# Optimization experiments

Hardware: AMD Instinct MI355X
Metric: run time of the kernel (lower is better)

Reference implementation:

```python
import jax, jax.numpy as jnp
import numpy as np

B, S, DMODEL, HEADS = 2, 2048, 1024, 16
DK = DMODEL // HEADS
DV = DMODEL // HEADS


def setup_inputs() -> dict:
    key = jax.random.key(0)
    kx, kq, kk, kv = jax.random.split(key, 4)
    x = jax.random.normal(kx, (B, S, DMODEL), dtype=jnp.float32)
    # stacked per-head projection weights, shape [H, dmodel, dk/dv]
    # (equivalent to nn.Linear(dmodel, dk, bias=False) per head)
    scale = 1.0 / np.sqrt(DMODEL)
    Wq = jax.random.uniform(kq, (HEADS, DMODEL, DK), jnp.float32, -scale, scale)
    Wk = jax.random.uniform(kk, (HEADS, DMODEL, DK), jnp.float32, -scale, scale)
    Wv = jax.random.uniform(kv, (HEADS, DMODEL, DV), jnp.float32, -scale, scale)
    return {"x": x, "Wq": Wq, "Wk": Wk, "Wv": Wv}


def reference(x, Wq, Wk, Wv):
    # per-head projections, batched across heads: [B,H,S,dk]
    q = jnp.einsum("bsd,hdk->bhsk", x, Wq)
    k = jnp.einsum("bsd,hdk->bhsk", x, Wk)
    v = jnp.einsum("bsd,hdv->bhsv", x, Wv)
    # NOTE: original module applies NO 1/sqrt(dk) scaling — keep faithful
    scores = jnp.einsum("bhqk,bhsk->bhqs", q, k)  # [B,H,S,S]
    attn = jax.nn.softmax(scores, axis=-1)
    out = jnp.einsum("bhqs,bhsv->bhqv", attn, v)  # [B,H,S,dv]
    # concat heads along last dim in head order
    Bsz, H, Sq, Dv = out.shape
    return jnp.transpose(out, (0, 2, 1, 3)).reshape(Bsz, Sq, H * Dv)
```

## Files before the change

kernel.cpp:

```cpp
#include <hip/hip_runtime.h>

#define B_ 2
#define S_ 2048
#define D_ 1024
#define H_ 16
#define DK_ 64
#define M_ (B_ * S_)
#define N_ (3 * D_)

typedef __bf16 bf16x8 __attribute__((ext_vector_type(8)));
typedef short s8vec __attribute__((ext_vector_type(8)));
typedef float f4vec __attribute__((ext_vector_type(4)));

static __device__ __forceinline__ ushort f2b(float f) {
  union { float f; unsigned u; } v; v.f = f;
  unsigned u = v.u;
  u += 0x7FFFu + ((u >> 16) & 1u);
  return (ushort)(u >> 16);
}

static __device__ __forceinline__ unsigned pk2(float a, float b) {
#if __has_builtin(__builtin_amdgcn_cvt_pk_bf16_f32)
  typedef __bf16 b2 __attribute__((ext_vector_type(2)));
  b2 r = __builtin_amdgcn_cvt_pk_bf16_f32(a, b);
  return __builtin_bit_cast(unsigned, r);
#else
  return (unsigned)f2b(a) | ((unsigned)f2b(b) << 16);
#endif
}

static __device__ __forceinline__ float exp2f_fast(float x) {
#if __has_builtin(__builtin_amdgcn_exp2f)
  return __builtin_amdgcn_exp2f(x);
#else
  return __expf(x * 0.6931471805599453f);
#endif
}

static __device__ __forceinline__ f4vec mfma16(s8vec a, s8vec b, f4vec c) {
  return __builtin_amdgcn_mfma_f32_16x16x32_bf16(
      __builtin_bit_cast(bf16x8, a), __builtin_bit_cast(bf16x8, b), c, 0, 0, 0);
}

static __device__ __forceinline__ void gl_lds16(const ushort* g, ushort* l) {
  __builtin_amdgcn_global_load_lds(
      (const __attribute__((address_space(1))) unsigned*)g,
      (__attribute__((address_space(3))) unsigned*)l, 16, 0, 0);
}

static __device__ __forceinline__ void wg_barrier_lds() {
  asm volatile("" ::: "memory");
  __builtin_amdgcn_s_waitcnt(0xC07F);
  __builtin_amdgcn_s_barrier();
  asm volatile("" ::: "memory");
}

__global__ __launch_bounds__(256) void cvt_xw(const float* __restrict__ x,
                                              const float* __restrict__ Wq,
                                              const float* __restrict__ Wk,
                                              const float* __restrict__ Wv,
                                              ushort* __restrict__ xb,
                                              ushort* __restrict__ wbt) {
  __shared__ ushort T[64 * 72];
  const int t = threadIdx.x;
  if (blockIdx.x < 4096) {
    int i = blockIdx.x * 256 + t;
    float4 v = ((const float4*)x)[i];
    ushort4 o;
    o.x = f2b(v.x); o.y = f2b(v.y); o.z = f2b(v.z); o.w = f2b(v.w);
    ((ushort4*)xb)[i] = o;
    return;
  }
  const int r = blockIdx.x - 4096;
  const int w = r >> 8, h = (r >> 4) & 15, d0 = (r & 15) * 64;
  const float* W = (w == 0) ? Wq : (w == 1) ? Wk : Wv;
  const float sc = (w == 0) ? 1.4426950408889634f : 1.0f;
  const float* src = W + (size_t)h * 65536 + (size_t)d0 * 64;
#pragma unroll
  for (int j = 0; j < 4; ++j) {
    int idx = j * 256 + t;
    int dr = idx >> 4, kc = (idx & 15) * 4;
    float4 v = *(const float4*)(src + dr * 64 + kc);
    T[(kc + 0) * 72 + dr] = f2b(v.x * sc);
    T[(kc + 1) * 72 + dr] = f2b(v.y * sc);
    T[(kc + 2) * 72 + dr] = f2b(v.z * sc);
    T[(kc + 3) * 72 + dr] = f2b(v.w * sc);
  }
  __syncthreads();
  const int kk = t >> 2, dcg = (t & 3) * 16;
  ushort* dst = wbt + ((size_t)w * 1024 + h * 64 + kk) * 1024 + d0 + dcg;
  *(s8vec*)dst       = *(const s8vec*)&T[kk * 72 + dcg];
  *(s8vec*)(dst + 8) = *(const s8vec*)&T[kk * 72 + dcg + 8];
}

__global__ __launch_bounds__(256) void proj_gemm(const ushort* __restrict__ xb,
                                                 const ushort* __restrict__ wbt,
                                                 ushort* __restrict__ qkv) {
  __shared__ __attribute__((aligned(16))) ushort As[128 * 64];
  __shared__ __attribute__((aligned(16))) ushort Bs[128 * 64];
  const int tid = threadIdx.x, wid = tid >> 6, lane = tid & 63;
  const int quad = lane >> 4, l15 = lane & 15;
  const int wm = wid & 1, wn = wid >> 1;
  const int m0 = blockIdx.x * 128, n0 = blockIdx.y * 128;

  f4vec acc[4][4];
#pragma unroll
  for (int mb = 0; mb < 4; mb++)
#pragma unroll
    for (int nb = 0; nb < 4; nb++)
#pragma unroll
      for (int i = 0; i < 4; i++) acc[mb][nb][i] = 0.f;

  const int sr = tid >> 3, sg = tid & 7;
  const int lg = sg ^ (sr & 7);
  const ushort* Ab = xb + (size_t)m0 * D_;
  const ushort* Bb = wbt + (size_t)n0 * D_;

  for (int k0 = 0; k0 < D_; k0 += 64) {
    __syncthreads();
#pragma unroll
    for (int j = 0; j < 4; ++j) {
      int r = j * 32 + sr;
      gl_lds16(Ab + (size_t)r * D_ + k0 + lg * 8, &As[j * 2048 + wid * 512]);
      gl_lds16(Bb + (size_t)r * D_ + k0 + lg * 8, &Bs[j * 2048 + wid * 512]);
    }
    __syncthreads();

#pragma unroll
    for (int kb = 0; kb < 2; ++kb) {
      s8vec af[4], bf[4];
#pragma unroll
      for (int mb = 0; mb < 4; ++mb) {
        int m = wm * 64 + mb * 16 + l15;
        int gpos = (kb * 4 + quad) ^ (m & 7);
        af[mb] = *(const s8vec*)&As[m * 64 + gpos * 8];
      }
#pragma unroll
      for (int nb = 0; nb < 4; ++nb) {
        int n = wn * 64 + nb * 16 + l15;
        int gpos = (kb * 4 + quad) ^ (n & 7);
        bf[nb] = *(const s8vec*)&Bs[n * 64 + gpos * 8];
      }
#pragma unroll
      for (int mb = 0; mb < 4; ++mb)
#pragma unroll
        for (int nb = 0; nb < 4; ++nb)
          acc[mb][nb] = mfma16(af[mb], bf[nb], acc[mb][nb]);
    }
  }

  const size_t per = (size_t)B_ * H_ * S_ * DK_;
  const int w = n0 >> 10;
  if (w == 2) {
    ushort* vt = qkv + 2 * per;
#pragma unroll
    for (int mb = 0; mb < 4; ++mb)
#pragma unroll
      for (int nb = 0; nb < 4; ++nb)
#pragma unroll
        for (int i = 0; i < 4; ++i) {
          int m = m0 + wm * 64 + mb * 16 + quad * 4 + i;
          int b = m >> 11, s = m & 2047;
          int n1 = (n0 & 1023) + wn * 64 + nb * 16 + l15;
          vt[((size_t)b * 1024 + n1) * S_ + s] = f2b(acc[mb][nb][i]);
        }
  } else {
#pragma unroll
    for (int mb = 0; mb < 4; ++mb)
#pragma unroll
      for (int nb = 0; nb < 4; ++nb)
#pragma unroll
        for (int i = 0; i < 4; ++i) {
          int m = m0 + wm * 64 + mb * 16 + quad * 4 + i;
          int b = m >> 11, s = m & 2047;
          int n1 = (n0 & 1023) + wn * 64 + nb * 16 + l15;
          qkv[(size_t)w * per + (((size_t)b * H_ + (n1 >> 6)) * S_ + s) * 64 + (n1 & 63)] =
              f2b(acc[mb][nb][i]);
        }
  }
}

__global__ __launch_bounds__(256) void attn(const ushort* __restrict__ qg,
                                            const ushort* __restrict__ kg,
                                            const ushort* __restrict__ vtg,
                                            float* __restrict__ out) {
  __shared__ __attribute__((aligned(16))) ushort Ks[128 * 64];
  __shared__ __attribute__((aligned(16))) ushort Vt[2][64 * 64];
  const int qt = blockIdx.x, bh = blockIdx.y;
  const int b = bh >> 4, h = bh & 15;
  const int tid = threadIdx.x, wid = tid >> 6, lane = tid & 63;
  const int quad = lane >> 4, l15 = lane & 15, l7 = l15 & 7;

  const ushort* qbase = qg + ((size_t)bh * S_ + qt * 128 + wid * 32) * DK_;
  s8vec bq[2][2];
#pragma unroll
  for (int qb = 0; qb < 2; ++qb)
#pragma unroll
    for (int kc = 0; kc < 2; ++kc)
      bq[qb][kc] = *(const s8vec*)(qbase + (size_t)(qb * 16 + l15) * DK_ + kc * 32 + quad * 8);

  f4vec o[4][2];
  float lsum[2] = {0.f, 0.f};
#pragma unroll
  for (int nb = 0; nb < 4; ++nb)
#pragma unroll
    for (int qb = 0; qb < 2; ++qb)
#pragma unroll
      for (int i = 0; i < 4; ++i) o[nb][qb][i] = 0.f;

  const int r5 = tid >> 3, gs = tid & 7;
  const int gk = gs ^ (r5 & 7);
  const ushort* kb_ = kg + (size_t)bh * S_ * DK_;
  const ushort* vb_ = vtg + (size_t)bh * 64 * S_;

  s8vec kr[4], vr[4];
#pragma unroll
  for (int j = 0; j < 4; ++j)
    kr[j] = *(const s8vec*)(kb_ + (size_t)(j * 32 + r5) * DK_ + gk * 8);
#pragma unroll
  for (int jd = 0; jd < 2; ++jd)
#pragma unroll
    for (int hf = 0; hf < 2; ++hf)
      vr[jd * 2 + hf] = *(const s8vec*)(vb_ + (size_t)(jd * 32 + r5) * S_ + hf * 64 + gk * 8);

#define LDAK(i, buf)                                                      \
  do {                                                                    \
    const int r0_ = ((i) * 2 + 0) * 16 + l15;                             \
    const int r1_ = ((i) * 2 + 1) * 16 + l15;                             \
    akb[buf][0] = *(const s8vec*)&Ks[r0_ * 64 + ((0 + quad) ^ l7) * 8];   \
    akb[buf][1] = *(const s8vec*)&Ks[r0_ * 64 + ((4 + quad) ^ l7) * 8];   \
    akb[buf][2] = *(const s8vec*)&Ks[r1_ * 64 + ((0 + quad) ^ l7) * 8];   \
    akb[buf][3] = *(const s8vec*)&Ks[r1_ * 64 + ((4 + quad) ^ l7) * 8];   \
  } while (0)

#define LDAV(i)                                                           \
  do {                                                                    \
    const int hf_ = (i) >> 1, G_ = ((i) & 1) * 4 + quad;                  \
    _Pragma("unroll")                                                     \
    for (int nb = 0; nb < 4; ++nb)                                        \
      avb[nb] = *(const s8vec*)&Vt[hf_][(nb * 16 + l15) * 64 + (G_ ^ l7) * 8]; \
  } while (0)

#define QKC(buf)                                                          \
  do {                                                                    \
    _Pragma("unroll")                                                     \
    for (int kbs = 0; kbs < 2; ++kbs)                                     \
      _Pragma("unroll")                                                   \
      for (int qb = 0; qb < 2; ++qb) {                                    \
        f4vec zz;                                                         \
        zz[0] = zz[1] = zz[2] = zz[3] = 0.f;                              \
        zz = mfma16(akb[buf][kbs * 2 + 0], bq[qb][0], zz);                \
        stb[buf][kbs][qb] = mfma16(akb[buf][kbs * 2 + 1], bq[qb][1], zz); \
      }                                                                   \
  } while (0)

#define SMPV(buf)                                                         \
  do {                                                                    \
    _Pragma("unroll")                                                     \
    for (int qb = 0; qb < 2; ++qb) {                                      \
      float p0 = exp2f_fast(stb[buf][0][qb][0]);                          \
      float p1 = exp2f_fast(stb[buf][0][qb][1]);                          \
      float p2 = exp2f_fast(stb[buf][0][qb][2]);                          \
      float p3 = exp2f_fast(stb[buf][0][qb][3]);                          \
      float p4 = exp2f_fast(stb[buf][1][qb][0]);                          \
      float p5 = exp2f_fast(stb[buf][1][qb][1]);                          \
      float p6 = exp2f_fast(stb[buf][1][qb][2]);                          \
      float p7 = exp2f_fast(stb[buf][1][qb][3]);                          \
      lsum[qb] += ((p0 + p1) + (p2 + p3)) + ((p4 + p5) + (p6 + p7));      \
      unsigned w0 = pk2(p0, p1), w1 = pk2(p2, p3);                        \
      unsigned w2 = pk2(p4, p5), w3 = pk2(p6, p7);                        \
      asm("v_permlane32_swap_b32 %0, %1" : "+v"(w0), "+v"(w2));           \
      asm("v_permlane16_swap_b32 %0, %1" : "+v"(w0), "+v"(w2));           \
      asm("v_permlane32_swap_b32 %0, %1" : "+v"(w1), "+v"(w3));           \
      asm("v_permlane16_swap_b32 %0, %1" : "+v"(w1), "+v"(w3));           \
      union { unsigned u[4]; s8vec v; } pb;                               \
      pb.u[0] = w0; pb.u[1] = w1; pb.u[2] = w2; pb.u[3] = w3;             \
      _Pragma("unroll")                                                   \
      for (int nb = 0; nb < 4; ++nb)                                      \
        o[nb][qb] = mfma16(avb[nb], pb.v, o[nb][qb]);                     \
    }                                                                     \
  } while (0)

  for (int kt = 0; kt < S_ / 128; ++kt) {
    wg_barrier_lds();
#pragma unroll
    for (int j = 0; j < 4; ++j)
      *(s8vec*)&Ks[(j * 32 + r5) * 64 + gs * 8] = kr[j];
#pragma unroll
    for (int jd = 0; jd < 2; ++jd)
#pragma unroll
      for (int hf = 0; hf < 2; ++hf)
        *(s8vec*)&Vt[hf][(jd * 32 + r5) * 64 + gs * 8] = vr[jd * 2 + hf];
    if (kt + 1 < S_ / 128) {
      const ushort* kn = kb_ + (size_t)(kt + 1) * 128 * DK_;
#pragma unroll
      for (int j = 0; j < 4; ++j)
        kr[j] = *(const s8vec*)(kn + (size_t)(j * 32 + r5) * DK_ + gk * 8);
      const ushort* vn = vb_ + (kt + 1) * 128;
#pragma unroll
      for (int jd = 0; jd < 2; ++jd)
#pragma unroll
        for (int hf = 0; hf < 2; ++hf)
          vr[jd * 2 + hf] = *(const s8vec*)(vn + (size_t)(jd * 32 + r5) * S_ + hf * 64 + gk * 8);
    }
    wg_barrier_lds();

    s8vec akb[2][4];
    s8vec avb[4];
    f4vec stb[2][2][2];

    LDAK(0, 0);
    LDAV(0);
    LDAK(1, 1);
    QKC(0);
#pragma unroll
    for (int i = 0; i < 4; ++i) {
      const int cur = i & 1, nxt = cur ^ 1;
      if (i < 2) LDAK(i + 2, cur);
      if (i < 3) QKC(nxt);
      SMPV(cur);
      if (i < 3) LDAV(i + 1);
    }
  }
#undef LDAK
#undef LDAV
#undef QKC
#undef SMPV

  float inv[2];
#pragma unroll
  for (int qb = 0; qb < 2; ++qb) {
    float s = lsum[qb];
    s += __shfl_xor(s, 16, 64);
    s += __shfl_xor(s, 32, 64);
    inv[qb] = 1.0f / s;
  }

  float* ob = out + ((size_t)b * S_ + qt * 128 + wid * 32) * D_ + h * DK_;
#pragma unroll
  for (int qb = 0; qb < 2; ++qb)
#pragma unroll
    for (int nb = 0; nb < 4; ++nb) {
      float4 vvv;
      vvv.x = o[nb][qb][0] * inv[qb];
      vvv.y = o[nb][qb][1] * inv[qb];
      vvv.z = o[nb][qb][2] * inv[qb];
      vvv.w = o[nb][qb][3] * inv[qb];
      *(float4*)&ob[(size_t)(qb * 16 + l15) * D_ + nb * 16 + quad * 4] = vvv;
    }
}

extern "C" void kernel_launch(void* const* d_in, const int* in_sizes, int n_in,
                              void* d_out, int out_size, void* d_ws, size_t ws_size,
                              hipStream_t stream) {
  const float* x  = (const float*)d_in[0];
  const float* Wq = (const float*)d_in[1];
  const float* Wk = (const float*)d_in[2];
  const float* Wv = (const float*)d_in[3];
  float* out = (float*)d_out;

  ushort* xb  = (ushort*)d_ws;
  ushort* wbt = xb + (size_t)B_ * S_ * D_;
  ushort* qkv = wbt + (size_t)3 * D_ * D_;
  const size_t per = (size_t)B_ * H_ * S_ * DK_;

  cvt_xw<<<4096 + 768, 256, 0, stream>>>(x, Wq, Wk, Wv, xb, wbt);
  proj_gemm<<<dim3(M_ / 128, N_ / 128), 256, 0, stream>>>(xb, wbt, qkv);
  attn<<<dim3(S_ / 128, B_ * H_), 256, 0, stream>>>(qkv, qkv + per, qkv + 2 * per, out);
}
```

Baseline: 174.8 us.

## Double-buffer projection GEMM with larger 256x192 tiles and 512 threads

The projection GEMM now uses 256x192 output tiles computed by 8 waves, each wave holding an 8x3 grid of MFMA accumulators. Shared-memory staging is double-buffered, so the global-to-LDS load for the next K step is issued before computing the current one, and only one barrier remains per iteration. The aim is to hide global load latency and raise operand reuse per LDS byte. The cost is a larger LDS footprint (about 112KB) and more accumulator registers, which lowers occupancy. The grid drops to 16x16 blocks, and because tiles can straddle the Q/K/V boundary, the Q/K versus transposed-V write choice is now made per column.

```diff
diff --git a/kernel.cpp b/kernel.cpp
--- a/kernel.cpp
+++ b/kernel.cpp
@@ -93,91 +93,103 @@
   *(s8vec*)(dst + 8) = *(const s8vec*)&T[kk * 72 + dcg + 8];
 }
 
-__global__ __launch_bounds__(256) void proj_gemm(const ushort* __restrict__ xb,
+__global__ __launch_bounds__(512) void proj_gemm(const ushort* __restrict__ xb,
                                                  const ushort* __restrict__ wbt,
                                                  ushort* __restrict__ qkv) {
-  __shared__ __attribute__((aligned(16))) ushort As[128 * 64];
-  __shared__ __attribute__((aligned(16))) ushort Bs[128 * 64];
+  __shared__ __attribute__((aligned(16))) ushort As[2][256 * 64];
+  __shared__ __attribute__((aligned(16))) ushort Bs[2][192 * 64];
   const int tid = threadIdx.x, wid = tid >> 6, lane = tid & 63;
   const int quad = lane >> 4, l15 = lane & 15;
   const int wm = wid & 1, wn = wid >> 1;
-  const int m0 = blockIdx.x * 128, n0 = blockIdx.y * 128;
-
-  f4vec acc[4][4];
-#pragma unroll
-  for (int mb = 0; mb < 4; mb++)
-#pragma unroll
-    for (int nb = 0; nb < 4; nb++)
+  const int m0 = blockIdx.x * 256, n0 = blockIdx.y * 192;
+
+  f4vec acc[8][3];
+#pragma unroll
+  for (int mb = 0; mb < 8; mb++)
+#pragma unroll
+    for (int nb = 0; nb < 3; nb++)
 #pragma unroll
       for (int i = 0; i < 4; i++) acc[mb][nb][i] = 0.f;
 
   const int sr = tid >> 3, sg = tid & 7;
-  const int lg = sg ^ (sr & 7);
+  const int gk = sg ^ (sr & 7);
   const ushort* Ab = xb + (size_t)m0 * D_;
   const ushort* Bb = wbt + (size_t)n0 * D_;
 
-  for (int k0 = 0; k0 < D_; k0 += 64) {
+#define PSTAGE(buf, k0_)                                                    \
+  do {                                                                      \
+    _Pragma("unroll")                                                       \
+    for (int j = 0; j < 4; ++j)                                             \
+      gl_lds16(Ab + (size_t)(j * 64 + sr) * D_ + (k0_) + gk * 8,            \
+               &As[buf][(j * 64 + wid * 8) * 64]);                          \
+    _Pragma("unroll")                                                       \
+    for (int j = 0; j < 3; ++j)                                             \
+      gl_lds16(Bb + (size_t)(j * 64 + sr) * D_ + (k0_) + gk * 8,            \
+               &Bs[buf][(j * 64 + wid * 8) * 64]);                          \
+  } while (0)
+
+#define PCOMP(buf)                                                          \
+  do {                                                                      \
+    _Pragma("unroll")                                                       \
+    for (int kb = 0; kb < 2; ++kb) {                                        \
+      s8vec af[8], bf[3];                                                   \
+      _Pragma("unroll")                                                     \
+      for (int mb = 0; mb < 8; ++mb) {                                      \
+        int m = wm * 128 + mb * 16 + l15;                                   \
+        int gpos = (kb * 4 + quad) ^ (m & 7);                               \
+        af[mb] = *(const s8vec*)&As[buf][m * 64 + gpos * 8];                \
+      }                                                                     \
+      _Pragma("unroll")                                                     \
+      for (int nb = 0; nb < 3; ++nb) {                                      \
+        int n = wn * 48 + nb * 16 + l15;                                    \
+        int gpos = (kb * 4 + quad) ^ (n & 7);                               \
+        bf[nb] = *(const s8vec*)&Bs[buf][n * 64 + gpos * 8];                \
+      }                                                                     \
+      _Pragma("unroll")                                                     \
+      for (int mb = 0; mb < 8; ++mb)                                        \
+        _Pragma("unroll")                                                   \
+        for (int nb = 0; nb < 3; ++nb)                                      \
+          acc[mb][nb] = mfma16(af[mb], bf[nb], acc[mb][nb]);                \
+    }                                                                       \
+  } while (0)
+
+  PSTAGE(0, 0);
+  __syncthreads();
+  for (int t = 0; t < 15; ++t) {
+    const int cur = t & 1;
+    PSTAGE(cur ^ 1, (t + 1) * 64);
+    PCOMP(cur);
     __syncthreads();
-#pragma unroll
-    for (int j = 0; j < 4; ++j) {
-      int r = j * 32 + sr;
-      gl_lds16(Ab + (size_t)r * D_ + k0 + lg * 8, &As[j * 2048 + wid * 512]);
-      gl_lds16(Bb + (size_t)r * D_ + k0 + lg * 8, &Bs[j * 2048 + wid * 512]);
-    }
-    __syncthreads();
-
-#pragma unroll
-    for (int kb = 0; kb < 2; ++kb) {
-      s8vec af[4], bf[4];
-#pragma unroll
-      for (int mb = 0; mb < 4; ++mb) {
-        int m = wm * 64 + mb * 16 + l15;
-        int gpos = (kb * 4 + quad) ^ (m & 7);
-        af[mb] = *(const s8vec*)&As[m * 64 + gpos * 8];
-      }
-#pragma unroll
-      for (int nb = 0; nb < 4; ++nb) {
-        int n = wn * 64 + nb * 16 + l15;
-        int gpos = (kb * 4 + quad) ^ (n & 7);
-        bf[nb] = *(const s8vec*)&Bs[n * 64 + gpos * 8];
-      }
-#pragma unroll
-      for (int mb = 0; mb < 4; ++mb)
-#pragma unroll
-        for (int nb = 0; nb < 4; ++nb)
-          acc[mb][nb] = mfma16(af[mb], bf[nb], acc[mb][nb]);
-    }
-  }
+  }
+  PCOMP(1);
+#undef PSTAGE
+#undef PCOMP
 
   const size_t per = (size_t)B_ * H_ * S_ * DK_;
-  const int w = n0 >> 10;
-  if (w == 2) {
-    ushort* vt = qkv + 2 * per;
-#pragma unroll
-    for (int mb = 0; mb < 4; ++mb)
-#pragma unroll
-      for (int nb = 0; nb < 4; ++nb)
+  ushort* vt = qkv + 2 * per;
+#pragma unroll
+  for (int mb = 0; mb < 8; ++mb)
+#pragma unroll
+    for (int nb = 0; nb < 3; ++nb) {
+      const int n1g = n0 + wn * 48 + nb * 16 + l15;
+      const int w = n1g >> 10, n1 = n1g & 1023;
+      if (w == 2) {
 #pragma unroll
         for (int i = 0; i < 4; ++i) {
-          int m = m0 + wm * 64 + mb * 16 + quad * 4 + i;
+          int m = m0 + wm * 128 + mb * 16 + quad * 4 + i;
           int b = m >> 11, s = m & 2047;
-          int n1 = (n0 & 1023) + wn * 64 + nb * 16 + l15;
           vt[((size_t)b * 1024 + n1) * S_ + s] = f2b(acc[mb][nb][i]);
         }
-  } else {
-#pragma unroll
-    for (int mb = 0; mb < 4; ++mb)
-#pragma unroll
-      for (int nb = 0; nb < 4; ++nb)
+      } else {
 #pragma unroll
         for (int i = 0; i < 4; ++i) {
-          int m = m0 + wm * 64 + mb * 16 + quad * 4 + i;
+          int m = m0 + wm * 128 + mb * 16 + quad * 4 + i;
           int b = m >> 11, s = m & 2047;
-          int n1 = (n0 & 1023) + wn * 64 + nb * 16 + l15;
           qkv[(size_t)w * per + (((size_t)b * H_ + (n1 >> 6)) * S_ + s) * 64 + (n1 & 63)] =
               f2b(acc[mb][nb][i]);
         }
-  }
+      }
+    }
 }
 
 __global__ __launch_bounds__(256) void attn(const ushort* __restrict__ qg,
@@ -365,6 +377,6 @@
   const size_t per = (size_t)B_ * H_ * S_ * DK_;
 
   cvt_xw<<<4096 + 768, 256, 0, stream>>>(x, Wq, Wk, Wv, xb, wbt);
-  proj_gemm<<<dim3(M_ / 128, N_ / 128), 256, 0, stream>>>(xb, wbt, qkv);
+  proj_gemm<<<dim3(M_ / 256, N_ / 192), 512, 0, stream>>>(xb, wbt, qkv);
   attn<<<dim3(S_ / 128, B_ * H_), 256, 0, stream>>>(qkv, qkv + per, qkv + 2 * per, out);
 }
```

Result: faster. 166.8 us (-4.6%).
